# Optimization experiments

Measured on AMD Instinct MI355X. Metric: run time of the kernel, lower is better.

## Reference

```python
import jax, jax.numpy as jnp
import numpy as np

N, D = 8192, 512
SPARSITY = 0.05  # fraction of nonzero entries in originalMatrix
EPS = 1e-12      # torch F.normalize eps


def setup_inputs() -> dict:
    key = jax.random.key(0)
    k1, k2, k3 = jax.random.split(key, 3)
    vals = jax.random.normal(k1, (N, N), dtype=jnp.float32)
    keep = jax.random.uniform(k2, (N, N)) < SPARSITY
    originalMatrix = jnp.where(keep, vals, 0.0)
    featureMatrix = jax.random.normal(k3, (N, D), dtype=jnp.float32)
    return {"originalMatrix": originalMatrix, "featureMatrix": featureMatrix}


def reference(originalMatrix, featureMatrix):
    # L2-normalize rows (torch.nn.functional.normalize, p=2, dim=1)
    norm = jnp.sqrt(jnp.sum(featureMatrix * featureMatrix, axis=1, keepdims=True))
    f = featureMatrix / jnp.maximum(norm, EPS)
    # dense cosine-similarity matrix [N, N]
    new_adj = jnp.matmul(f, f.T)
    # MSE over only the nonzero entries of originalMatrix (the Python double-loop)
    mask = originalMatrix != 0
    diff = jnp.where(mask, originalMatrix - new_adj, 0.0)
    count = jnp.sum(mask).astype(new_adj.dtype)
    return jnp.sum(diff * diff) / count
```

## Files before the change

### kernel.cpp

```cpp
#include <hip/hip_runtime.h>
#include <hip/hip_bf16.h>

#define N_DIM 8192
#define D_DIM 512
#define BM 128
#define BN 128
#define BK 64
#define NTILES 2080

typedef float f32x4 __attribute__((ext_vector_type(4)));
typedef short bf16x8 __attribute__((ext_vector_type(8)));
typedef unsigned int u32;

__global__ __launch_bounds__(256) void normalize_rows_k(
    const float* __restrict__ feat, __hip_bfloat16* __restrict__ fb)
{
    const int w    = threadIdx.x >> 6;
    const int lane = threadIdx.x & 63;
    const int row  = blockIdx.x * 4 + w;

    const float* src = feat + (size_t)row * D_DIM + lane * 8;
    float4 v0 = *reinterpret_cast<const float4*>(src);
    float4 v1 = *reinterpret_cast<const float4*>(src + 4);

    float ss = v0.x*v0.x + v0.y*v0.y + v0.z*v0.z + v0.w*v0.w
             + v1.x*v1.x + v1.y*v1.y + v1.z*v1.z + v1.w*v1.w;
    #pragma unroll
    for (int off = 32; off; off >>= 1) ss += __shfl_xor(ss, off);

    const float r = 1.0f / fmaxf(sqrtf(ss), 1e-12f);

    union { ushort u[8]; uint4 q; } pk;
    float vals[8] = { v0.x, v0.y, v0.z, v0.w, v1.x, v1.y, v1.z, v1.w };
    #pragma unroll
    for (int i = 0; i < 8; ++i) {
        __hip_bfloat16 b = __float2bfloat16(vals[i] * r);
        pk.u[i] = *reinterpret_cast<ushort*>(&b);
    }
    *reinterpret_cast<uint4*>(fb + (size_t)row * D_DIM + lane * 8) = pk.q;
}

__global__ __launch_bounds__(256, 3) void fused_gemm_loss_k(
    const __hip_bfloat16* __restrict__ fb,
    const float* __restrict__ orig,
    float* __restrict__ partials)
{
    __shared__ __align__(16) __hip_bfloat16 As[BM * BK];
    __shared__ __align__(16) __hip_bfloat16 Bs[BN * BK];
    __shared__ float red[8];

    int b = blockIdx.x, br = 0;
    while (b >= 64 - br) { b -= 64 - br; ++br; }
    const int bc  = br + b;
    const int tr0 = br * BM;
    const int tc0 = bc * BN;

    const int tid  = threadIdx.x;
    const int w    = tid >> 6;
    const int lane = tid & 63;
    const int wr   = w >> 1;
    const int wc   = w & 1;
    const int fr   = lane & 15;
    const int rsub = (lane >> 4) * 4;

    f32x4 acc[4][4] = {};

    const int srow  = lane >> 3;
    const int scols = (((lane & 7) ^ (lane >> 3)) * 8);

    for (int k0 = 0; k0 < D_DIM; k0 += BK) {
        #pragma unroll
        for (int t = 0; t < 4; ++t) {
            const int c = w * 4 + t;
            const int rowA = tr0 + c * 8 + srow;
            const int rowB = tc0 + c * 8 + srow;
            const __hip_bfloat16* gA = fb + (size_t)rowA * D_DIM + k0 + scols;
            const __hip_bfloat16* gB = fb + (size_t)rowB * D_DIM + k0 + scols;
            __builtin_amdgcn_global_load_lds(
                (const __attribute__((address_space(1))) u32*)gA,
                (__attribute__((address_space(3))) u32*)(As + c * 512),
                16, 0, 0);
            __builtin_amdgcn_global_load_lds(
                (const __attribute__((address_space(1))) u32*)gB,
                (__attribute__((address_space(3))) u32*)(Bs + c * 512),
                16, 0, 0);
        }
        __syncthreads();

        const int krow = lane >> 4;
        const int sw   = (fr & 7) << 4;
        #pragma unroll
        for (int kk = 0; kk < BK; kk += 32) {
            bf16x8 af[4], bfr[4];
            #pragma unroll
            for (int fm = 0; fm < 4; ++fm) {
                const int r = wr * 64 + fm * 16 + fr;
                af[fm] = *reinterpret_cast<const bf16x8*>(
                    (const char*)As + r * 128 + (((kk << 1) + (krow << 4)) ^ sw));
            }
            #pragma unroll
            for (int fn = 0; fn < 4; ++fn) {
                const int r = wc * 64 + fn * 16 + fr;
                bfr[fn] = *reinterpret_cast<const bf16x8*>(
                    (const char*)Bs + r * 128 + (((kk << 1) + (krow << 4)) ^ sw));
            }
            #pragma unroll
            for (int fm = 0; fm < 4; ++fm)
                #pragma unroll
                for (int fn = 0; fn < 4; ++fn)
                    acc[fm][fn] = __builtin_amdgcn_mfma_f32_16x16x32_bf16(
                        af[fm], bfr[fn], acc[fm][fn], 0, 0, 0);
        }
        __syncthreads();
    }

    float lsum = 0.0f, lcnt = 0.0f;

    #pragma unroll
    for (int fm = 0; fm < 4; ++fm) {
        #pragma unroll
        for (int v = 0; v < 4; ++v) {
            const int row = tr0 + wr * 64 + fm * 16 + rsub + v;
            const float* orow = orig + (size_t)row * N_DIM + tc0 + wc * 64;
            #pragma unroll
            for (int fn = 0; fn < 4; ++fn) {
                const float o = orow[fn * 16 + fr];
                if (o != 0.0f) {
                    const float d = o - acc[fm][fn][v];
                    lsum += d * d;
                    lcnt += 1.0f;
                }
            }
        }
    }

    if (br != bc) {
        #pragma unroll
        for (int fm = 0; fm < 4; ++fm) {
            const int rbase = tr0 + wr * 64 + fm * 16 + rsub;
            #pragma unroll
            for (int fn = 0; fn < 4; ++fn) {
                const int col = tc0 + wc * 64 + fn * 16 + fr;
                const float4 o4 = *reinterpret_cast<const float4*>(
                    orig + (size_t)col * N_DIM + rbase);
                const float ov[4] = { o4.x, o4.y, o4.z, o4.w };
                #pragma unroll
                for (int v = 0; v < 4; ++v) {
                    if (ov[v] != 0.0f) {
                        const float d = ov[v] - acc[fm][fn][v];
                        lsum += d * d;
                        lcnt += 1.0f;
                    }
                }
            }
        }
    }

    #pragma unroll
    for (int off = 32; off; off >>= 1) {
        lsum += __shfl_xor(lsum, off);
        lcnt += __shfl_xor(lcnt, off);
    }
    if (lane == 0) { red[w * 2] = lsum; red[w * 2 + 1] = lcnt; }
    __syncthreads();
    if (tid == 0) {
        float s = 0.0f, c = 0.0f;
        #pragma unroll
        for (int i = 0; i < 4; ++i) { s += red[i * 2]; c += red[i * 2 + 1]; }
        partials[(size_t)blockIdx.x * 2]     = s;
        partials[(size_t)blockIdx.x * 2 + 1] = c;
    }
}

__global__ __launch_bounds__(256) void final_reduce_k(
    const float* __restrict__ partials, float* __restrict__ out, int nb)
{
    __shared__ float rs[4], rc[4];
    float s = 0.0f, c = 0.0f;
    for (int i = threadIdx.x; i < nb; i += 256) {
        s += partials[(size_t)i * 2];
        c += partials[(size_t)i * 2 + 1];
    }
    #pragma unroll
    for (int off = 32; off; off >>= 1) {
        s += __shfl_xor(s, off);
        c += __shfl_xor(c, off);
    }
    const int w = threadIdx.x >> 6, lane = threadIdx.x & 63;
    if (lane == 0) { rs[w] = s; rc[w] = c; }
    __syncthreads();
    if (threadIdx.x == 0) {
        const float S = rs[0] + rs[1] + rs[2] + rs[3];
        const float C = rc[0] + rc[1] + rc[2] + rc[3];
        out[0] = S / C;
    }
}

extern "C" void kernel_launch(void* const* d_in, const int* in_sizes, int n_in,
                              void* d_out, int out_size, void* d_ws, size_t ws_size,
                              hipStream_t stream)
{
    const float* orig = (const float*)d_in[0];
    const float* feat = (const float*)d_in[1];
    float* out = (float*)d_out;

    __hip_bfloat16* fb = (__hip_bfloat16*)d_ws;
    float* partials = (float*)((char*)d_ws + (size_t)N_DIM * D_DIM * 2);

    normalize_rows_k<<<N_DIM / 4, 256, 0, stream>>>(feat, fb);
    fused_gemm_loss_k<<<NTILES, 256, 0, stream>>>(fb, orig, partials);
    final_reduce_k<<<1, 256, 0, stream>>>(partials, out, NTILES);
}
```

Before: 88.40 us.

## Fold final reduction into GEMM via fixed-point atomics, nontemporal loads, occupancy 4

Removes the separate final reduction kernel: each tile block atomically adds fixed-point sums and counts into 64-bit counters, and the last block to finish computes the result. The accumulator is zeroed in the normalize kernel. The loads of originalMatrix become nontemporal, and launch bounds ask for four blocks per CU instead of three. This saves a kernel launch and may improve cache behaviour and occupancy, at the cost of fixed-point quantization and possible register pressure.

```diff
diff --git a/kernel.cpp b/kernel.cpp
--- a/kernel.cpp
+++ b/kernel.cpp
@@ -11,10 +11,14 @@
 typedef float f32x4 __attribute__((ext_vector_type(4)));
 typedef short bf16x8 __attribute__((ext_vector_type(8)));
 typedef unsigned int u32;
+typedef unsigned long long u64;
 
 __global__ __launch_bounds__(256) void normalize_rows_k(
-    const float* __restrict__ feat, __hip_bfloat16* __restrict__ fb)
+    const float* __restrict__ feat, __hip_bfloat16* __restrict__ fb,
+    u64* __restrict__ accum)
 {
+    if (blockIdx.x == 0 && threadIdx.x < 3) accum[threadIdx.x] = 0ull;
+
     const int w    = threadIdx.x >> 6;
     const int lane = threadIdx.x & 63;
     const int row  = blockIdx.x * 4 + w;
@@ -40,10 +44,11 @@
     *reinterpret_cast<uint4*>(fb + (size_t)row * D_DIM + lane * 8) = pk.q;
 }
 
-__global__ __launch_bounds__(256, 3) void fused_gemm_loss_k(
+__global__ __launch_bounds__(256, 4) void fused_gemm_loss_k(
     const __hip_bfloat16* __restrict__ fb,
     const float* __restrict__ orig,
-    float* __restrict__ partials)
+    u64* __restrict__ accum,
+    float* __restrict__ out)
 {
     __shared__ __align__(16) __hip_bfloat16 As[BM * BK];
     __shared__ __align__(16) __hip_bfloat16 Bs[BN * BK];
@@ -124,7 +129,7 @@
             const float* orow = orig + (size_t)row * N_DIM + tc0 + wc * 64;
             #pragma unroll
             for (int fn = 0; fn < 4; ++fn) {
-                const float o = orow[fn * 16 + fr];
+                const float o = __builtin_nontemporal_load(orow + fn * 16 + fr);
                 if (o != 0.0f) {
                     const float d = o - acc[fm][fn][v];
                     lsum += d * d;
@@ -141,13 +146,12 @@
             #pragma unroll
             for (int fn = 0; fn < 4; ++fn) {
                 const int col = tc0 + wc * 64 + fn * 16 + fr;
-                const float4 o4 = *reinterpret_cast<const float4*>(
-                    orig + (size_t)col * N_DIM + rbase);
-                const float ov[4] = { o4.x, o4.y, o4.z, o4.w };
+                const f32x4 o4 = __builtin_nontemporal_load(
+                    reinterpret_cast<const f32x4*>(orig + (size_t)col * N_DIM + rbase));
                 #pragma unroll
                 for (int v = 0; v < 4; ++v) {
-                    if (ov[v] != 0.0f) {
-                        const float d = ov[v] - acc[fm][fn][v];
+                    if (o4[v] != 0.0f) {
+                        const float d = o4[v] - acc[fm][fn][v];
                         lsum += d * d;
                         lcnt += 1.0f;
                     }
@@ -167,32 +171,19 @@
         float s = 0.0f, c = 0.0f;
         #pragma unroll
         for (int i = 0; i < 4; ++i) { s += red[i * 2]; c += red[i * 2 + 1]; }
-        partials[(size_t)blockIdx.x * 2]     = s;
-        partials[(size_t)blockIdx.x * 2 + 1] = c;
-    }
-}
-
-__global__ __launch_bounds__(256) void final_reduce_k(
-    const float* __restrict__ partials, float* __restrict__ out, int nb)
-{
-    __shared__ float rs[4], rc[4];
-    float s = 0.0f, c = 0.0f;
-    for (int i = threadIdx.x; i < nb; i += 256) {
-        s += partials[(size_t)i * 2];
-        c += partials[(size_t)i * 2 + 1];
-    }
-    #pragma unroll
-    for (int off = 32; off; off >>= 1) {
-        s += __shfl_xor(s, off);
-        c += __shfl_xor(c, off);
-    }
-    const int w = threadIdx.x >> 6, lane = threadIdx.x & 63;
-    if (lane == 0) { rs[w] = s; rc[w] = c; }
-    __syncthreads();
-    if (threadIdx.x == 0) {
-        const float S = rs[0] + rs[1] + rs[2] + rs[3];
-        const float C = rc[0] + rc[1] + rc[2] + rc[3];
-        out[0] = S / C;
+
+        const u64 qs = (u64)((double)s * 4294967296.0);
+        const u64 qc = (u64)(c + 0.5f);
+        atomicAdd(&accum[0], qs);
+        atomicAdd(&accum[1], qc);
+        __threadfence();
+        const u64 done = atomicAdd(&accum[2], 1ull);
+        if (done == NTILES - 1) {
+            __threadfence();
+            const u64 S = atomicAdd(&accum[0], 0ull);
+            const u64 C = atomicAdd(&accum[1], 0ull);
+            out[0] = (float)(((double)S / 4294967296.0) / (double)C);
+        }
     }
 }
 
@@ -205,9 +196,8 @@
     float* out = (float*)d_out;
 
     __hip_bfloat16* fb = (__hip_bfloat16*)d_ws;
-    float* partials = (float*)((char*)d_ws + (size_t)N_DIM * D_DIM * 2);
-
-    normalize_rows_k<<<N_DIM / 4, 256, 0, stream>>>(feat, fb);
-    fused_gemm_loss_k<<<NTILES, 256, 0, stream>>>(fb, orig, partials);
-    final_reduce_k<<<1, 256, 0, stream>>>(partials, out, NTILES);
+    u64* accum = (u64*)((char*)d_ws + (size_t)N_DIM * D_DIM * 2);
+
+    normalize_rows_k<<<N_DIM / 4, 256, 0, stream>>>(feat, fb, accum);
+    fused_gemm_loss_k<<<NTILES, 256, 0, stream>>>(fb, orig, accum, out);
 }
```

Result: slower. 228.2 us (+158.1%).
